# Kernel optimization log

Hardware: AMD Instinct MI355X
Metric: run time of the kernel (lower is better)

## Reference

```python
import jax, jax.numpy as jnp
import numpy as np

B, S, D, H, DH = 2, 2048, 2048, 16, 128


def _rope(t, cos, sin):
    # t: [b,s,h,dh]; pairs are consecutive elements (view(..., -1, 2) in torch)
    te = t[..., 0::2]
    to = t[..., 1::2]
    re = te * cos - to * sin
    im = te * sin + to * cos
    return jnp.stack([re, im], axis=-1).reshape(t.shape)


def setup_inputs() -> dict:
    key = jax.random.key(0)
    ks = jax.random.split(key, 5)
    inv = 1.0 / np.sqrt(D)
    x = jax.random.normal(ks[0], (B, S, D), dtype=jnp.float32)
    # standard RoPE angle table -> cos/sin of shape [1,S,1,DH//2]
    pos = jnp.arange(S, dtype=jnp.float32)[:, None]
    freqs = 1.0 / (10000.0 ** (jnp.arange(0, DH, 2, dtype=jnp.float32) / DH))
    ang = pos * freqs[None, :]
    rope_cos = jnp.cos(ang)[None, :, None, :]
    rope_sin = jnp.sin(ang)[None, :, None, :]
    Wq = jax.random.normal(ks[1], (D, D), dtype=jnp.float32) * inv
    Wk = jax.random.normal(ks[2], (D, D), dtype=jnp.float32) * inv
    Wv = jax.random.normal(ks[3], (D, D), dtype=jnp.float32) * inv
    Wo = jax.random.normal(ks[4], (D, D), dtype=jnp.float32) * inv
    return {"x": x, "rope_cos": rope_cos, "rope_sin": rope_sin,
            "Wq": Wq, "Wk": Wk, "Wv": Wv, "Wo": Wo}


def reference(x, rope_cos, rope_sin, Wq, Wk, Wv, Wo):
    b, s, d = x.shape
    scale = DH ** (-0.5)
    # nn.Linear(bias=False): y = x @ W.T
    q = (x @ Wq.T).reshape(b, s, H, DH)
    k = (x @ Wk.T).reshape(b, s, H, DH)
    v = (x @ Wv.T).reshape(b, s, H, DH)
    q = _rope(q, rope_cos[:, :s], rope_sin[:, :s])
    k = _rope(k, rope_cos[:, :s], rope_sin[:, :s])
    q = q.transpose(0, 2, 1, 3)  # bhsd
    k = k.transpose(0, 2, 1, 3)
    v = v.transpose(0, 2, 1, 3)
    # full scores needed for softmax normalizer
    scores = jnp.einsum('bhqd,bhkd->bhqk', q, k) * scale
    lse = jax.nn.logsumexp(scores, axis=-1)  # [b,h,s]
    # torch.einsum('bhss,bhsd->bhsd', softmax(scores), v) takes the DIAGONAL
    # of the softmax matrix and scales v elementwise. Replicate exactly:
    diag = jnp.einsum('bhsd,bhsd->bhs', q, k) * scale  # scores[b,h,s,s]
    w = jnp.exp(diag - lse)  # softmax(scores)[b,h,s,s]
    out = w[..., None] * v  # [b,h,s,dh]
    out = out.transpose(0, 2, 1, 3).reshape(b, s, d)
    return out @ Wo.T
```

## Files before the change

kernel.cpp:

```cpp
#include <hip/hip_runtime.h>

#define B_  2
#define S_  2048
#define D_  2048
#define H_  16
#define DH_ 128
#define M_  (B_ * S_)

typedef __bf16 bf16;
typedef __bf16 bf16x2 __attribute__((ext_vector_type(2)));
typedef __bf16 bf16x4 __attribute__((ext_vector_type(4)));
typedef __bf16 bf16x8 __attribute__((ext_vector_type(8)));
typedef float  f32x4  __attribute__((ext_vector_type(4)));

#define EXP2F(x) __builtin_amdgcn_exp2f(x)
#define LOG2F(x) __builtin_amdgcn_logf(x)

static constexpr float kQScale = 0.08838834764831845f * 1.4426950408889634f;

__device__ __forceinline__ void async16(const void* g, void* l) {
  __builtin_amdgcn_global_load_lds(
      (const __attribute__((address_space(1))) void*)g,
      (__attribute__((address_space(3))) void*)l, 16, 0, 0);
}

__global__ void cvt_bf16(const float* __restrict__ s, bf16* __restrict__ d) {
  int i = (blockIdx.x * 256 + threadIdx.x) * 4;
  float4 v = *(const float4*)(s + i);
  bf16x4 o = {(bf16)v.x, (bf16)v.y, (bf16)v.z, (bf16)v.w};
  *(bf16x4*)(d + i) = o;
}

__global__ __launch_bounds__(256, 2) void gemm_qkv(
    const bf16* __restrict__ A, const bf16* __restrict__ Bm,
    const float* __restrict__ rc, const float* __restrict__ rs,
    bf16* __restrict__ qb, bf16* __restrict__ kb, bf16* __restrict__ vb) {
  __shared__ alignas(16) bf16 As[128 * 32];
  __shared__ alignas(16) bf16 Bs[128 * 32];
  const int tid = threadIdx.x;
  const int lane = tid & 63, wv = tid >> 6;
  const int quad = lane >> 4, c16 = lane & 15;
  const int wm = (wv >> 1) * 64, wn = (wv & 1) * 64;
  const int m0 = blockIdx.y * 128, n0 = blockIdx.x * 128;

  const bf16* ag = A  + (size_t)(m0 + (tid >> 2)) * D_ + (tid & 3) * 8;
  const bf16* bg = Bm + (size_t)(n0 + (tid >> 2)) * D_ + (tid & 3) * 8;
  char* asl = (char*)As + tid * 16;
  char* bsl = (char*)Bs + tid * 16;

  f32x4 acc[4][4] = {};
  for (int k0 = 0; k0 < D_; k0 += 32) {
    __syncthreads();
    async16(ag + k0,            asl);
    async16(ag + k0 + 64 * D_,  asl + 4096);
    async16(bg + k0,            bsl);
    async16(bg + k0 + 64 * D_,  bsl + 4096);
    __syncthreads();
    bf16x8 af[4], bfr[4];
#pragma unroll
    for (int i = 0; i < 4; ++i)
      af[i] = *(const bf16x8*)(As + (wm + i * 16 + c16) * 32 + quad * 8);
#pragma unroll
    for (int j = 0; j < 4; ++j)
      bfr[j] = *(const bf16x8*)(Bs + (wn + j * 16 + c16) * 32 + quad * 8);
#pragma unroll
    for (int i = 0; i < 4; ++i)
#pragma unroll
      for (int j = 0; j < 4; ++j)
        acc[i][j] = __builtin_amdgcn_mfma_f32_16x16x32_bf16(af[i], bfr[j], acc[i][j], 0, 0, 0);
  }

  if (n0 < 4096) {
    bf16* dst = (n0 < 2048) ? qb : kb;
    const float sc = (n0 < 2048) ? kQScale : 1.0f;
#pragma unroll
    for (int i = 0; i < 4; ++i) {
      const int gmi = m0 + wm + i * 16 + quad * 4;
#pragma unroll
      for (int j = 0; j < 4; ++j) {
        const int gn = n0 + wn + j * 16 + c16;
        const int h = (gn >> 7) & 15;
        const int d = gn & 127;
#pragma unroll
        for (int r = 0; r < 4; ++r) {
          float v = acc[i][j][r];
          float p = __shfl_xor(v, 1);
          const int gm = gmi + r;
          const int b = gm >> 11, s = gm & 2047;
          const int si = s * 64 + (d >> 1);
          float c = rc[si], sn = rs[si];
          float re = (v * c - p * sn) * sc;
          float im = (v * sn + p * c) * sc;
          if (!(lane & 1)) {
            bf16x2 o = {(bf16)re, (bf16)im};
            *(bf16x2*)(dst + ((size_t)((b * 16 + h) * 2048 + s) * 128 + d)) = o;
          }
        }
      }
    }
  } else {
#pragma unroll
    for (int i = 0; i < 4; ++i) {
      const int gmi = m0 + wm + i * 16 + quad * 4;
#pragma unroll
      for (int j = 0; j < 4; ++j) {
        const int gn = n0 + wn + j * 16 + c16 - 4096;
#pragma unroll
        for (int r = 0; r < 4; ++r) {
          float v = acc[i][j][r];
          float p = __shfl_xor(v, 1);
          if (!(lane & 1)) {
            bf16x2 o = {(bf16)v, (bf16)p};
            *(bf16x2*)(vb + (size_t)(gmi + r) * 2048 + gn) = o;
          }
        }
      }
    }
  }
}

__global__ __launch_bounds__(256, 2) void score_lse(
    const bf16* __restrict__ qb, const bf16* __restrict__ kb,
    float* __restrict__ lse, float* __restrict__ diag) {
  __shared__ alignas(16) bf16 Qs[4 * 128 * 32];
  __shared__ alignas(16) bf16 Ks[4 * 128 * 32];
  const int tid = threadIdx.x;
  const int lane = tid & 63, wv = tid >> 6;
  const int quad = lane >> 4, c16 = lane & 15;
  const int wm = wv * 32;
  const int bh = blockIdx.y;
  const int m0 = blockIdx.x * 128;
  const bf16* Q  = qb + (size_t)bh * (S_ * DH_);
  const bf16* Kp = kb + (size_t)bh * (S_ * DH_);

  const bf16* qg = Q + (size_t)(m0 + (tid >> 2)) * DH_ + (tid & 3) * 8;
  char* ql = (char*)Qs + tid * 16;
#pragma unroll
  for (int kt = 0; kt < 4; ++kt) {
    async16(qg + kt * 32,             ql + kt * 8192);
    async16(qg + kt * 32 + 64 * DH_,  ql + kt * 8192 + 4096);
  }

  const bf16* kg = Kp + (size_t)(tid >> 2) * DH_ + (tid & 3) * 8;
  char* kl = (char*)Ks + tid * 16;

  float sums[8] = {0.f, 0.f, 0.f, 0.f, 0.f, 0.f, 0.f, 0.f};

  for (int n0 = 0; n0 < S_; n0 += 128) {
    __syncthreads();
#pragma unroll
    for (int kt = 0; kt < 4; ++kt) {
      async16(kg + (size_t)n0 * DH_ + kt * 32,            kl + kt * 8192);
      async16(kg + (size_t)(n0 + 64) * DH_ + kt * 32,     kl + kt * 8192 + 4096);
    }
    __syncthreads();
    f32x4 acc[2][8] = {};
#pragma unroll
    for (int kt = 0; kt < 4; ++kt) {
      bf16x8 a[2], b[8];
#pragma unroll
      for (int i = 0; i < 2; ++i)
        a[i] = *(const bf16x8*)(Qs + kt * 4096 + (wm + i * 16 + c16) * 32 + quad * 8);
#pragma unroll
      for (int j = 0; j < 8; ++j)
        b[j] = *(const bf16x8*)(Ks + kt * 4096 + (j * 16 + c16) * 32 + quad * 8);
#pragma unroll
      for (int i = 0; i < 2; ++i)
#pragma unroll
        for (int j = 0; j < 8; ++j)
          acc[i][j] = __builtin_amdgcn_mfma_f32_16x16x32_bf16(a[i], b[j], acc[i][j], 0, 0, 0);
    }
    if (n0 == m0) {
#pragma unroll
      for (int i = 0; i < 2; ++i)
#pragma unroll
        for (int j = 0; j < 8; ++j)
          if (j == 2 * wv + i) {
#pragma unroll
            for (int r = 0; r < 4; ++r)
              if (c16 == quad * 4 + r) {
                int row = wm + i * 16 + quad * 4 + r;
                diag[bh * S_ + m0 + row] = acc[i][j][r];
              }
          }
    }
#pragma unroll
    for (int i = 0; i < 2; ++i)
#pragma unroll
      for (int j = 0; j < 8; ++j)
#pragma unroll
        for (int r = 0; r < 4; ++r)
          sums[i * 4 + r] += EXP2F(acc[i][j][r]);
  }

#pragma unroll
  for (int t = 0; t < 8; ++t) {
    float s = sums[t];
    s += __shfl_xor(s, 1);
    s += __shfl_xor(s, 2);
    s += __shfl_xor(s, 4);
    s += __shfl_xor(s, 8);
    if (c16 == 0) {
      int i = t >> 2, r = t & 3;
      lse[bh * S_ + m0 + wm + i * 16 + quad * 4 + r] = LOG2F(s);
    }
  }
}

__global__ void wv_mul(const bf16* __restrict__ vb, const float* __restrict__ lse,
                       const float* __restrict__ diag, bf16* __restrict__ t) {
  int u = blockIdx.x * 256 + threadIdx.x;
  int e = u * 8;
  int m = e >> 11;
  int c = e & 2047;
  int g = ((m >> 11) * 16 + (c >> 7)) * 2048 + (m & 2047);
  float w = EXP2F(diag[g] - lse[g]);
  bf16x8 v = ((const bf16x8*)vb)[u];
  bf16x8 o;
#pragma unroll
  for (int r = 0; r < 8; ++r) o[r] = (bf16)((float)v[r] * w);
  ((bf16x8*)t)[u] = o;
}

__global__ __launch_bounds__(256, 2) void gemm_out(
    const bf16* __restrict__ A, const bf16* __restrict__ Bm, float* __restrict__ C) {
  __shared__ alignas(16) bf16 As[128 * 32];
  __shared__ alignas(16) bf16 Bs[128 * 32];
  const int tid = threadIdx.x;
  const int lane = tid & 63, wv = tid >> 6;
  const int quad = lane >> 4, c16 = lane & 15;
  const int wm = (wv >> 1) * 64, wn = (wv & 1) * 64;
  const int m0 = blockIdx.y * 128, n0 = blockIdx.x * 128;

  const bf16* ag = A  + (size_t)(m0 + (tid >> 2)) * D_ + (tid & 3) * 8;
  const bf16* bg = Bm + (size_t)(n0 + (tid >> 2)) * D_ + (tid & 3) * 8;
  char* asl = (char*)As + tid * 16;
  char* bsl = (char*)Bs + tid * 16;

  f32x4 acc[4][4] = {};
  for (int k0 = 0; k0 < D_; k0 += 32) {
    __syncthreads();
    async16(ag + k0,            asl);
    async16(ag + k0 + 64 * D_,  asl + 4096);
    async16(bg + k0,            bsl);
    async16(bg + k0 + 64 * D_,  bsl + 4096);
    __syncthreads();
    bf16x8 af[4], bfr[4];
#pragma unroll
    for (int i = 0; i < 4; ++i)
      af[i] = *(const bf16x8*)(As + (wm + i * 16 + c16) * 32 + quad * 8);
#pragma unroll
    for (int j = 0; j < 4; ++j)
      bfr[j] = *(const bf16x8*)(Bs + (wn + j * 16 + c16) * 32 + quad * 8);
#pragma unroll
    for (int i = 0; i < 4; ++i)
#pragma unroll
      for (int j = 0; j < 4; ++j)
        acc[i][j] = __builtin_amdgcn_mfma_f32_16x16x32_bf16(af[i], bfr[j], acc[i][j], 0, 0, 0);
  }
#pragma unroll
  for (int i = 0; i < 4; ++i)
#pragma unroll
    for (int j = 0; j < 4; ++j)
#pragma unroll
      for (int r = 0; r < 4; ++r) {
        float v = acc[i][j][r];
        float p = __shfl_xor(v, 1);
        if (!(lane & 1)) {
          int gm = m0 + wm + i * 16 + quad * 4 + r;
          int gn = n0 + wn + j * 16 + c16;
          float2 o = {v, p};
          *(float2*)(C + (size_t)gm * D_ + gn) = o;
        }
      }
}

extern "C" void kernel_launch(void* const* d_in, const int* in_sizes, int n_in,
                              void* d_out, int out_size, void* d_ws, size_t ws_size,
                              hipStream_t stream) {
  (void)in_sizes; (void)n_in; (void)out_size; (void)ws_size;
  const float* x  = (const float*)d_in[0];
  const float* rc = (const float*)d_in[1];
  const float* rs = (const float*)d_in[2];
  const float* Wq = (const float*)d_in[3];
  const float* Wk = (const float*)d_in[4];
  const float* Wv = (const float*)d_in[5];
  const float* Wo = (const float*)d_in[6];

  char* ws = (char*)d_ws;
  bf16* xb   = (bf16*)ws;
  bf16* wqkv = (bf16*)(ws + 16777216);
  bf16* wob  = (bf16*)(ws + 16777216 + 25165824);
  bf16* qb   = (bf16*)(ws + 16777216 + 25165824 + 8388608);
  bf16* kb   = qb + 8388608;
  bf16* vb   = kb + 8388608;
  float* lse = (float*)(vb + 8388608);
  float* dia = lse + 65536;

  cvt_bf16<<<8192, 256, 0, stream>>>(x,  xb);
  cvt_bf16<<<4096, 256, 0, stream>>>(Wq, wqkv);
  cvt_bf16<<<4096, 256, 0, stream>>>(Wk, wqkv + 4194304);
  cvt_bf16<<<4096, 256, 0, stream>>>(Wv, wqkv + 8388608);
  cvt_bf16<<<4096, 256, 0, stream>>>(Wo, wob);

  gemm_qkv<<<dim3(48, 32), 256, 0, stream>>>(xb, wqkv, rc, rs, qb, kb, vb);
  score_lse<<<dim3(16, 32), 256, 0, stream>>>(qb, kb, lse, dia);
  wv_mul<<<4096, 256, 0, stream>>>(vb, lse, dia, xb );
  gemm_out<<<dim3(16, 32), 256, 0, stream>>>(xb, wob, (float*)d_out);
}
```

Before: 392.2 us.

## Store fused QKV row-major and load 64-wide K chunks per GEMM barrier

```diff
diff --git a/kernel.cpp b/kernel.cpp
--- a/kernel.cpp
+++ b/kernel.cpp
@@ -5,7 +5,7 @@
 #define D_  2048
 #define H_  16
 #define DH_ 128
-#define M_  (B_ * S_)
+#define NQKV 6144
 
 typedef __bf16 bf16;
 typedef __bf16 bf16x2 __attribute__((ext_vector_type(2)));
@@ -34,11 +34,12 @@
 __global__ __launch_bounds__(256, 2) void gemm_qkv(
     const bf16* __restrict__ A, const bf16* __restrict__ Bm,
     const float* __restrict__ rc, const float* __restrict__ rs,
-    bf16* __restrict__ qb, bf16* __restrict__ kb, bf16* __restrict__ vb) {
-  __shared__ alignas(16) bf16 As[128 * 32];
-  __shared__ alignas(16) bf16 Bs[128 * 32];
+    bf16* __restrict__ C) {
+  __shared__ alignas(16) bf16 As[2][128 * 32];
+  __shared__ alignas(16) bf16 Bs[2][128 * 32];
   const int tid = threadIdx.x;
-  const int lane = tid & 63, wv = tid >> 6;
+  const int lane = tid & 63;
+  const int wv = tid >> 6;
   const int quad = lane >> 4, c16 = lane & 15;
   const int wm = (wv >> 1) * 64, wn = (wv & 1) * 64;
   const int m0 = blockIdx.y * 128, n0 = blockIdx.x * 128;
@@ -49,29 +50,35 @@
   char* bsl = (char*)Bs + tid * 16;
 
   f32x4 acc[4][4] = {};
-  for (int k0 = 0; k0 < D_; k0 += 32) {
-    __syncthreads();
-    async16(ag + k0,            asl);
-    async16(ag + k0 + 64 * D_,  asl + 4096);
-    async16(bg + k0,            bsl);
-    async16(bg + k0 + 64 * D_,  bsl + 4096);
-    __syncthreads();
-    bf16x8 af[4], bfr[4];
-#pragma unroll
-    for (int i = 0; i < 4; ++i)
-      af[i] = *(const bf16x8*)(As + (wm + i * 16 + c16) * 32 + quad * 8);
-#pragma unroll
-    for (int j = 0; j < 4; ++j)
-      bfr[j] = *(const bf16x8*)(Bs + (wn + j * 16 + c16) * 32 + quad * 8);
-#pragma unroll
-    for (int i = 0; i < 4; ++i)
+  for (int k0 = 0; k0 < D_; k0 += 64) {
+    __syncthreads();
+    async16(ag + k0,                 asl);
+    async16(ag + k0 + 64 * D_,       asl + 4096);
+    async16(ag + k0 + 32,            asl + 8192);
+    async16(ag + k0 + 32 + 64 * D_,  asl + 12288);
+    async16(bg + k0,                 bsl);
+    async16(bg + k0 + 64 * D_,       bsl + 4096);
+    async16(bg + k0 + 32,            bsl + 8192);
+    async16(bg + k0 + 32 + 64 * D_,  bsl + 12288);
+    __syncthreads();
+#pragma unroll
+    for (int half = 0; half < 2; ++half) {
+      bf16x8 af[4], bfr[4];
+#pragma unroll
+      for (int i = 0; i < 4; ++i)
+        af[i] = *(const bf16x8*)(As[half] + (wm + i * 16 + c16) * 32 + quad * 8);
 #pragma unroll
       for (int j = 0; j < 4; ++j)
-        acc[i][j] = __builtin_amdgcn_mfma_f32_16x16x32_bf16(af[i], bfr[j], acc[i][j], 0, 0, 0);
+        bfr[j] = *(const bf16x8*)(Bs[half] + (wn + j * 16 + c16) * 32 + quad * 8);
+#pragma unroll
+      for (int i = 0; i < 4; ++i)
+#pragma unroll
+        for (int j = 0; j < 4; ++j)
+          acc[i][j] = __builtin_amdgcn_mfma_f32_16x16x32_bf16(af[i], bfr[j], acc[i][j], 0, 0, 0);
+    }
   }
 
   if (n0 < 4096) {
-    bf16* dst = (n0 < 2048) ? qb : kb;
     const float sc = (n0 < 2048) ? kQScale : 1.0f;
 #pragma unroll
     for (int i = 0; i < 4; ++i) {
@@ -79,21 +86,20 @@
 #pragma unroll
       for (int j = 0; j < 4; ++j) {
         const int gn = n0 + wn + j * 16 + c16;
-        const int h = (gn >> 7) & 15;
         const int d = gn & 127;
 #pragma unroll
         for (int r = 0; r < 4; ++r) {
           float v = acc[i][j][r];
           float p = __shfl_xor(v, 1);
           const int gm = gmi + r;
-          const int b = gm >> 11, s = gm & 2047;
+          const int s = gm & 2047;
           const int si = s * 64 + (d >> 1);
           float c = rc[si], sn = rs[si];
           float re = (v * c - p * sn) * sc;
           float im = (v * sn + p * c) * sc;
           if (!(lane & 1)) {
             bf16x2 o = {(bf16)re, (bf16)im};
-            *(bf16x2*)(dst + ((size_t)((b * 16 + h) * 2048 + s) * 128 + d)) = o;
+            *(bf16x2*)(C + (size_t)gm * NQKV + gn) = o;
           }
         }
       }
@@ -104,14 +110,14 @@
       const int gmi = m0 + wm + i * 16 + quad * 4;
 #pragma unroll
       for (int j = 0; j < 4; ++j) {
-        const int gn = n0 + wn + j * 16 + c16 - 4096;
+        const int gn = n0 + wn + j * 16 + c16;
 #pragma unroll
         for (int r = 0; r < 4; ++r) {
           float v = acc[i][j][r];
           float p = __shfl_xor(v, 1);
           if (!(lane & 1)) {
             bf16x2 o = {(bf16)v, (bf16)p};
-            *(bf16x2*)(vb + (size_t)(gmi + r) * 2048 + gn) = o;
+            *(bf16x2*)(C + (size_t)(gmi + r) * NQKV + gn) = o;
           }
         }
       }
@@ -120,7 +126,7 @@
 }
 
 __global__ __launch_bounds__(256, 2) void score_lse(
-    const bf16* __restrict__ qb, const bf16* __restrict__ kb,
+    const bf16* __restrict__ qkv,
     float* __restrict__ lse, float* __restrict__ diag) {
   __shared__ alignas(16) bf16 Qs[4 * 128 * 32];
   __shared__ alignas(16) bf16 Ks[4 * 128 * 32];
@@ -129,19 +135,20 @@
   const int quad = lane >> 4, c16 = lane & 15;
   const int wm = wv * 32;
   const int bh = blockIdx.y;
+  const int b = bh >> 4, h = bh & 15;
   const int m0 = blockIdx.x * 128;
-  const bf16* Q  = qb + (size_t)bh * (S_ * DH_);
-  const bf16* Kp = kb + (size_t)bh * (S_ * DH_);
-
-  const bf16* qg = Q + (size_t)(m0 + (tid >> 2)) * DH_ + (tid & 3) * 8;
+
+  const bf16* qg = qkv + (size_t)(b * 2048 + m0 + (tid >> 2)) * NQKV
+                 + h * 128 + (tid & 3) * 8;
   char* ql = (char*)Qs + tid * 16;
 #pragma unroll
   for (int kt = 0; kt < 4; ++kt) {
-    async16(qg + kt * 32,             ql + kt * 8192);
-    async16(qg + kt * 32 + 64 * DH_,  ql + kt * 8192 + 4096);
-  }
-
-  const bf16* kg = Kp + (size_t)(tid >> 2) * DH_ + (tid & 3) * 8;
+    async16(qg + kt * 32,               ql + kt * 8192);
+    async16(qg + kt * 32 + (size_t)64 * NQKV, ql + kt * 8192 + 4096);
+  }
+
+  const bf16* kg = qkv + (size_t)(b * 2048 + (tid >> 2)) * NQKV
+                 + 2048 + h * 128 + (tid & 3) * 8;
   char* kl = (char*)Ks + tid * 16;
 
   float sums[8] = {0.f, 0.f, 0.f, 0.f, 0.f, 0.f, 0.f, 0.f};
@@ -150,25 +157,25 @@
     __syncthreads();
 #pragma unroll
     for (int kt = 0; kt < 4; ++kt) {
-      async16(kg + (size_t)n0 * DH_ + kt * 32,            kl + kt * 8192);
-      async16(kg + (size_t)(n0 + 64) * DH_ + kt * 32,     kl + kt * 8192 + 4096);
+      async16(kg + (size_t)n0 * NQKV + kt * 32,        kl + kt * 8192);
+      async16(kg + (size_t)(n0 + 64) * NQKV + kt * 32, kl + kt * 8192 + 4096);
     }
     __syncthreads();
     f32x4 acc[2][8] = {};
 #pragma unroll
     for (int kt = 0; kt < 4; ++kt) {
-      bf16x8 a[2], b[8];
+      bf16x8 a[2], bb[8];
 #pragma unroll
       for (int i = 0; i < 2; ++i)
         a[i] = *(const bf16x8*)(Qs + kt * 4096 + (wm + i * 16 + c16) * 32 + quad * 8);
 #pragma unroll
       for (int j = 0; j < 8; ++j)
-        b[j] = *(const bf16x8*)(Ks + kt * 4096 + (j * 16 + c16) * 32 + quad * 8);
+        bb[j] = *(const bf16x8*)(Ks + kt * 4096 + (j * 16 + c16) * 32 + quad * 8);
 #pragma unroll
       for (int i = 0; i < 2; ++i)
 #pragma unroll
         for (int j = 0; j < 8; ++j)
-          acc[i][j] = __builtin_amdgcn_mfma_f32_16x16x32_bf16(a[i], b[j], acc[i][j], 0, 0, 0);
+          acc[i][j] = __builtin_amdgcn_mfma_f32_16x16x32_bf16(a[i], bb[j], acc[i][j], 0, 0, 0);
     }
     if (n0 == m0) {
 #pragma unroll
@@ -207,7 +214,7 @@
   }
 }
 
-__global__ void wv_mul(const bf16* __restrict__ vb, const float* __restrict__ lse,
+__global__ void wv_mul(const bf16* __restrict__ qkv, const float* __restrict__ lse,
                        const float* __restrict__ diag, bf16* __restrict__ t) {
   int u = blockIdx.x * 256 + threadIdx.x;
   int e = u * 8;
@@ -215,7 +222,7 @@
   int c = e & 2047;
   int g = ((m >> 11) * 16 + (c >> 7)) * 2048 + (m & 2047);
   float w = EXP2F(diag[g] - lse[g]);
-  bf16x8 v = ((const bf16x8*)vb)[u];
+  bf16x8 v = *(const bf16x8*)(qkv + (size_t)m * NQKV + 4096 + c);
   bf16x8 o;
 #pragma unroll
   for (int r = 0; r < 8; ++r) o[r] = (bf16)((float)v[r] * w);
@@ -224,8 +231,8 @@
 
 __global__ __launch_bounds__(256, 2) void gemm_out(
     const bf16* __restrict__ A, const bf16* __restrict__ Bm, float* __restrict__ C) {
-  __shared__ alignas(16) bf16 As[128 * 32];
-  __shared__ alignas(16) bf16 Bs[128 * 32];
+  __shared__ alignas(16) bf16 As[2][128 * 32];
+  __shared__ alignas(16) bf16 Bs[2][128 * 32];
   const int tid = threadIdx.x;
   const int lane = tid & 63, wv = tid >> 6;
   const int quad = lane >> 4, c16 = lane & 15;
@@ -238,25 +245,32 @@
   char* bsl = (char*)Bs + tid * 16;
 
   f32x4 acc[4][4] = {};
-  for (int k0 = 0; k0 < D_; k0 += 32) {
-    __syncthreads();
-    async16(ag + k0,            asl);
-    async16(ag + k0 + 64 * D_,  asl + 4096);
-    async16(bg + k0,            bsl);
-    async16(bg + k0 + 64 * D_,  bsl + 4096);
-    __syncthreads();
-    bf16x8 af[4], bfr[4];
-#pragma unroll
-    for (int i = 0; i < 4; ++i)
-      af[i] = *(const bf16x8*)(As + (wm + i * 16 + c16) * 32 + quad * 8);
-#pragma unroll
-    for (int j = 0; j < 4; ++j)
-      bfr[j] = *(const bf16x8*)(Bs + (wn + j * 16 + c16) * 32 + quad * 8);
-#pragma unroll
-    for (int i = 0; i < 4; ++i)
+  for (int k0 = 0; k0 < D_; k0 += 64) {
+    __syncthreads();
+    async16(ag + k0,                 asl);
+    async16(ag + k0 + 64 * D_,       asl + 4096);
+    async16(ag + k0 + 32,            asl + 8192);
+    async16(ag + k0 + 32 + 64 * D_,  asl + 12288);
+    async16(bg + k0,                 bsl);
+    async16(bg + k0 + 64 * D_,       bsl + 4096);
+    async16(bg + k0 + 32,            bsl + 8192);
+    async16(bg + k0 + 32 + 64 * D_,  bsl + 12288);
+    __syncthreads();
+#pragma unroll
+    for (int half = 0; half < 2; ++half) {
+      bf16x8 af[4], bfr[4];
+#pragma unroll
+      for (int i = 0; i < 4; ++i)
+        af[i] = *(const bf16x8*)(As[half] + (wm + i * 16 + c16) * 32 + quad * 8);
 #pragma unroll
       for (int j = 0; j < 4; ++j)
-        acc[i][j] = __builtin_amdgcn_mfma_f32_16x16x32_bf16(af[i], bfr[j], acc[i][j], 0, 0, 0);
+        bfr[j] = *(const bf16x8*)(Bs[half] + (wn + j * 16 + c16) * 32 + quad * 8);
+#pragma unroll
+      for (int i = 0; i < 4; ++i)
+#pragma unroll
+        for (int j = 0; j < 4; ++j)
+          acc[i][j] = __builtin_amdgcn_mfma_f32_16x16x32_bf16(af[i], bfr[j], acc[i][j], 0, 0, 0);
+    }
   }
 #pragma unroll
   for (int i = 0; i < 4; ++i)
@@ -291,10 +305,8 @@
   bf16* xb   = (bf16*)ws;
   bf16* wqkv = (bf16*)(ws + 16777216);
   bf16* wob  = (bf16*)(ws + 16777216 + 25165824);
-  bf16* qb   = (bf16*)(ws + 16777216 + 25165824 + 8388608);
-  bf16* kb   = qb + 8388608;
-  bf16* vb   = kb + 8388608;
-  float* lse = (float*)(vb + 8388608);
+  bf16* qkv  = (bf16*)(ws + 16777216 + 25165824 + 8388608);
+  float* lse = (float*)((char*)qkv + 50331648);
   float* dia = lse + 65536;
 
   cvt_bf16<<<8192, 256, 0, stream>>>(x,  xb);
@@ -303,8 +315,8 @@
   cvt_bf16<<<4096, 256, 0, stream>>>(Wv, wqkv + 8388608);
   cvt_bf16<<<4096, 256, 0, stream>>>(Wo, wob);
 
-  gemm_qkv<<<dim3(48, 32), 256, 0, stream>>>(xb, wqkv, rc, rs, qb, kb, vb);
-  score_lse<<<dim3(16, 32), 256, 0, stream>>>(qb, kb, lse, dia);
-  wv_mul<<<4096, 256, 0, stream>>>(vb, lse, dia, xb );
+  gemm_qkv<<<dim3(48, 32), 256, 0, stream>>>(xb, wqkv, rc, rs, qkv);
+  score_lse<<<dim3(16, 32), 256, 0, stream>>>(qkv, lse, dia);
+  wv_mul<<<4096, 256, 0, stream>>>(qkv, lse, dia, xb );
   gemm_out<<<dim3(16, 32), 256, 0, stream>>>(xb, wob, (float*)d_out);
 }
```

Measured after the change: 384.4 us. 1.02x faster.
